# Kernel tuning notes

Hardware: AMD Instinct MI355X
Metric: run time of the kernel (lower is better)

Reference implementation:

```python
import jax, jax.numpy as jnp
import numpy as np

S, B, D, HID, OUT = 96, 16, 512, 128, 2


def setup_inputs() -> dict:
    key = jax.random.key(0)
    ks = jax.random.split(key, 6)
    embeds = jax.random.normal(ks[0], (S, B, D), dtype=jnp.float32)
    embeds_cmp = jax.random.normal(ks[1], (S, B, D), dtype=jnp.float32)
    umask = jnp.ones((B, S), dtype=jnp.float32)   # unused by the math
    qmask = jnp.zeros((S, B, 2), dtype=jnp.float32)  # unused by the math
    # fc: Linear(2*D -> HID); classify: Linear(HID -> OUT)
    W1 = jax.random.normal(ks[2], (HID, 2 * D), dtype=jnp.float32) * 0.02
    b1 = jnp.zeros((HID,), dtype=jnp.float32)
    W2 = jax.random.normal(ks[3], (OUT, HID), dtype=jnp.float32) * 0.02
    b2 = jnp.zeros((OUT,), dtype=jnp.float32)
    return {"embeds": embeds, "umask": umask, "qmask": qmask,
            "embeds_cmp": embeds_cmp, "W1": W1, "b1": b1, "W2": W2, "b2": b2}


def reference(embeds, umask, qmask, embeds_cmp, W1, b1, W2, b2):
    # Pairwise concat [embeds_i ; embeds_cmp_j] -> Linear(2D->HID).
    # Split W1 into halves so the quadratic concat is never materialized:
    # concat(x1,x2) @ W1^T == x1 @ W1a^T + x2 @ W1b^T (same math, fused form).
    d = embeds.shape[-1]
    W1a, W1b = W1[:, :d], W1[:, d:]
    ha = jnp.einsum('ibd,hd->ibh', embeds, W1a)        # [S,B,HID]
    hb = jnp.einsum('jbd,hd->jbh', embeds_cmp, W1b)    # [S,B,HID]
    h = jax.nn.relu(ha[:, None] + hb[None, :] + b1)    # [S,S,B,HID]
    # Dropout(p=0.9) is identity in eval mode.
    logits = jnp.einsum('ijbh,ch->ijbc', h, W2) + b2   # [S,S,B,2]
    return logits
```

## Files before the change

### kernel.cpp

```cpp
#include <hip/hip_runtime.h>

#define S_   96
#define B_   16
#define D_   512
#define HID_ 128
#define M_   (S_ * B_)
#define KC_  4
#define KCH_ (D_ / KC_)
#define CHF_ (2 * M_ * HID_)

typedef __attribute__((ext_vector_type(4))) float        f32x4_t;
typedef __attribute__((ext_vector_type(2))) float        f32x2_t;
typedef __attribute__((ext_vector_type(4))) unsigned int u32x4_t;
typedef __attribute__((ext_vector_type(8))) short        short8;

static __device__ __forceinline__ void split8(f32x4_t a, f32x4_t b,
                                              short8& hi, short8& lo) {
    float f[8];
    #pragma unroll
    for (int j = 0; j < 4; ++j) { f[j] = a[j]; f[4 + j] = b[j]; }
    unsigned int hb[8], lb[8];
    #pragma unroll
    for (int j = 0; j < 8; ++j) {
        unsigned int u = __float_as_uint(f[j]);
        float hf = __uint_as_float(u & 0xffff0000u);
        hb[j] = u >> 16;
        lb[j] = __float_as_uint(f[j] - hf) >> 16;
    }
    union { u32x4_t u; short8 s; } H, L;
    #pragma unroll
    for (int j = 0; j < 4; ++j) {
        H.u[j] = hb[2 * j] | (hb[2 * j + 1] << 16);
        L.u[j] = lb[2 * j] | (lb[2 * j + 1] << 16);
    }
    hi = H.s; lo = L.s;
}

__global__ __launch_bounds__(256) void stage1_mfma(
    const float* __restrict__ emb,
    const float* __restrict__ embc,
    const float* __restrict__ W1,
    const float* __restrict__ b1,
    float* __restrict__ ws)
{
    __shared__ float x_s[64 * 132];
    __shared__ float w_s[64 * 132];

    const int t    = threadIdx.x;
    const int wave = t >> 6;
    const int lane = t & 63;
    const int bx   = blockIdx.x;
    const int h0   = blockIdx.y * 64;
    const int kc   = blockIdx.z;

    const int z    = (bx >= 24) ? 1 : 0;
    const int mloc = bx * 64 - z * M_;

    const float* xbase = (z ? embc : emb) + (size_t)mloc * D_ + kc * KCH_;
    const float* wbase = W1 + (size_t)h0 * (2 * D_) + z * D_ + kc * KCH_;

    #pragma unroll
    for (int rep = 0; rep < 8; ++rep) {
        const int idx = rep * 256 + t;
        const int row = idx >> 5;
        const int c4  = (idx & 31) * 4;
        *(f32x4_t*)&x_s[row * 132 + c4] = *(const f32x4_t*)(xbase + row * D_ + c4);
        *(f32x4_t*)&w_s[row * 132 + c4] = *(const f32x4_t*)(wbase + row * (2 * D_) + c4);
    }
    __syncthreads();

    const int rsel = lane & 15;
    const int kq   = (lane >> 4) * 8;
    const int wm   = (wave & 1) * 32;
    const int wh   = (wave >> 1) * 32;

    f32x4_t acc[2][2] = {{{0.f,0.f,0.f,0.f},{0.f,0.f,0.f,0.f}},
                         {{0.f,0.f,0.f,0.f},{0.f,0.f,0.f,0.f}}};
    #pragma unroll
    for (int kk = 0; kk < KCH_; kk += 32) {
        short8 ahi[2], alo[2], bhi[2], blo[2];
        #pragma unroll
        for (int ms = 0; ms < 2; ++ms) {
            const float* p = &x_s[(wm + ms * 16 + rsel) * 132 + kk + kq];
            split8(*(const f32x4_t*)p, *(const f32x4_t*)(p + 4), ahi[ms], alo[ms]);
        }
        #pragma unroll
        for (int hs = 0; hs < 2; ++hs) {
            const float* p = &w_s[(wh + hs * 16 + rsel) * 132 + kk + kq];
            split8(*(const f32x4_t*)p, *(const f32x4_t*)(p + 4), bhi[hs], blo[hs]);
        }
        #pragma unroll
        for (int ms = 0; ms < 2; ++ms)
            #pragma unroll
            for (int hs = 0; hs < 2; ++hs) {
                acc[ms][hs] = __builtin_amdgcn_mfma_f32_16x16x32_bf16(ahi[ms], bhi[hs], acc[ms][hs], 0, 0, 0);
                acc[ms][hs] = __builtin_amdgcn_mfma_f32_16x16x32_bf16(ahi[ms], blo[hs], acc[ms][hs], 0, 0, 0);
                acc[ms][hs] = __builtin_amdgcn_mfma_f32_16x16x32_bf16(alo[ms], bhi[hs], acc[ms][hs], 0, 0, 0);
            }
    }

    float* dst = ws + (size_t)kc * CHF_ + (size_t)z * (M_ * HID_);
    const int mrow_base = mloc + wm + (lane >> 4) * 4;
    #pragma unroll
    for (int ms = 0; ms < 2; ++ms) {
        #pragma unroll
        for (int hs = 0; hs < 2; ++hs) {
            const int h = h0 + wh + hs * 16 + rsel;
            const float bias = (z == 0 && kc == 0) ? b1[h] : 0.f;
            #pragma unroll
            for (int r = 0; r < 4; ++r) {
                dst[(mrow_base + ms * 16 + r) * HID_ + h] = acc[ms][hs][r] + bias;
            }
        }
    }
}

__global__ __launch_bounds__(256) void stage2(
    const float* __restrict__ ws,
    const float* __restrict__ W2,
    const float* __restrict__ b2,
    float* __restrict__ out)
{
    __shared__ float ha_s[16 * 132];
    __shared__ float hb_s[16 * 132];
    __shared__ float w2_s[2 * HID_];

    const int t  = threadIdx.x;
    const int i0 = blockIdx.x * 16;
    const int j0 = blockIdx.y * 16;
    const int b  = blockIdx.z;

    {
        const int r = t >> 4;
        const int c = (t & 15) * 8;
        const float* pHa = ws + ((i0 + r) * B_ + b) * HID_ + c;
        const float* pHb = ws + (M_ * HID_) + ((j0 + r) * B_ + b) * HID_ + c;
        f32x4_t a0 = *(const f32x4_t*)pHa,  a1  = *(const f32x4_t*)(pHa + 4);
        f32x4_t b0 = *(const f32x4_t*)pHb,  b1v = *(const f32x4_t*)(pHb + 4);
        #pragma unroll
        for (int kc = 1; kc < KC_; ++kc) {
            const float* qa = pHa + (size_t)kc * CHF_;
            const float* qb = pHb + (size_t)kc * CHF_;
            a0  += *(const f32x4_t*)qa;   a1  += *(const f32x4_t*)(qa + 4);
            b0  += *(const f32x4_t*)qb;   b1v += *(const f32x4_t*)(qb + 4);
        }
        *(f32x4_t*)&ha_s[r * 132 + c]     = a0;
        *(f32x4_t*)&ha_s[r * 132 + c + 4] = a1;
        *(f32x4_t*)&hb_s[r * 132 + c]     = b0;
        *(f32x4_t*)&hb_s[r * 132 + c + 4] = b1v;
        w2_s[t] = W2[t];
    }
    __syncthreads();

    const int ti = t >> 4, tj = t & 15;
    const float* pa = &ha_s[ti * 132];
    const float* pb = &hb_s[tj * 132];
    float acc0 = 0.f, acc1 = 0.f;
    #pragma unroll
    for (int h = 0; h < HID_; h += 4) {
        f32x4_t av = *(const f32x4_t*)(pa + h);
        f32x4_t bv = *(const f32x4_t*)(pb + h);
        f32x4_t w0 = *(const f32x4_t*)&w2_s[h];
        f32x4_t w1 = *(const f32x4_t*)&w2_s[HID_ + h];
        #pragma unroll
        for (int q = 0; q < 4; ++q) {
            float v = fmaxf(av[q] + bv[q], 0.f);
            acc0 = fmaf(v, w0[q], acc0);
            acc1 = fmaf(v, w1[q], acc1);
        }
    }

    const int i = i0 + ti, j = j0 + tj;
    const int idx = ((i * S_ + j) * B_ + b) * 2;
    f32x2_t o = { acc0 + b2[0], acc1 + b2[1] };
    *(f32x2_t*)(out + idx) = o;
}

__global__ __launch_bounds__(256) void fused_fallback(
    const float* __restrict__ emb,
    const float* __restrict__ embc,
    const float* __restrict__ W1,
    const float* __restrict__ b1,
    const float* __restrict__ W2,
    const float* __restrict__ b2,
    float* __restrict__ out)
{
    __shared__ float ha_s[16 * 132];
    __shared__ float hb_s[16 * 132];
    __shared__ float w2_s[2 * HID_];

    const int t  = threadIdx.x;
    const int i0 = blockIdx.x * 16;
    const int j0 = blockIdx.y * 16;
    const int b  = blockIdx.z;

    w2_s[t] = W2[t];

    for (int o = t; o < 4096; o += 256) {
        const int side = o >> 11;
        const int mi   = (o >> 7) & 15;
        const int h    = o & 127;
        const int srow = ((side ? j0 : i0) + mi) * B_ + b;
        const float* x = (side ? embc : emb) + srow * D_;
        const float* w = W1 + h * (2 * D_) + side * D_;
        float s = side ? 0.f : b1[h];
        for (int d = 0; d < D_; d += 4) {
            f32x4_t xv = *(const f32x4_t*)(x + d);
            f32x4_t wv = *(const f32x4_t*)(w + d);
            s = fmaf(xv[0], wv[0], s);
            s = fmaf(xv[1], wv[1], s);
            s = fmaf(xv[2], wv[2], s);
            s = fmaf(xv[3], wv[3], s);
        }
        (side ? hb_s : ha_s)[mi * 132 + h] = s;
    }
    __syncthreads();

    const int ti = t >> 4, tj = t & 15;
    const float* pa = &ha_s[ti * 132];
    const float* pb = &hb_s[tj * 132];
    float acc0 = 0.f, acc1 = 0.f;
    #pragma unroll
    for (int h = 0; h < HID_; h += 4) {
        f32x4_t av = *(const f32x4_t*)(pa + h);
        f32x4_t bv = *(const f32x4_t*)(pb + h);
        f32x4_t w0 = *(const f32x4_t*)&w2_s[h];
        f32x4_t w1 = *(const f32x4_t*)&w2_s[HID_ + h];
        #pragma unroll
        for (int q = 0; q < 4; ++q) {
            float v = fmaxf(av[q] + bv[q], 0.f);
            acc0 = fmaf(v, w0[q], acc0);
            acc1 = fmaf(v, w1[q], acc1);
        }
    }
    const int i = i0 + ti, j = j0 + tj;
    const int idx = ((i * S_ + j) * B_ + b) * 2;
    f32x2_t ov = { acc0 + b2[0], acc1 + b2[1] };
    *(f32x2_t*)(out + idx) = ov;
}

extern "C" void kernel_launch(void* const* d_in, const int* in_sizes, int n_in,
                              void* d_out, int out_size, void* d_ws, size_t ws_size,
                              hipStream_t stream) {
    const float* emb  = (const float*)d_in[0];
    const float* embc = (const float*)d_in[3];
    const float* W1   = (const float*)d_in[4];
    const float* b1   = (const float*)d_in[5];
    const float* W2   = (const float*)d_in[6];
    const float* b2   = (const float*)d_in[7];
    float* out = (float*)d_out;

    const size_t need = (size_t)KC_ * CHF_ * sizeof(float);
    if (d_ws != nullptr && ws_size >= need) {
        float* ws = (float*)d_ws;
        stage1_mfma<<<dim3(48, 2, KC_), 256, 0, stream>>>(emb, embc, W1, b1, ws);
        stage2<<<dim3(6, 6, 16), 256, 0, stream>>>(ws, W2, b2, out);
    } else {
        fused_fallback<<<dim3(6, 6, 16), 256, 0, stream>>>(emb, embc, W1, b1, W2, b2, out);
    }
}
```

Measured before the change: 88.21 us.

## Pre-split fp32 tiles into bf16 hi/lo in LDS; read W2 directly from global

```diff
diff --git a/kernel.cpp b/kernel.cpp
--- a/kernel.cpp
+++ b/kernel.cpp
@@ -8,6 +8,7 @@
 #define KC_  4
 #define KCH_ (D_ / KC_)
 #define CHF_ (2 * M_ * HID_)
+#define LSTR_ 136
 
 typedef __attribute__((ext_vector_type(4))) float        f32x4_t;
 typedef __attribute__((ext_vector_type(2))) float        f32x2_t;
@@ -43,8 +44,10 @@
     const float* __restrict__ b1,
     float* __restrict__ ws)
 {
-    __shared__ float x_s[64 * 132];
-    __shared__ float w_s[64 * 132];
+    __shared__ short x_hi[64 * LSTR_];
+    __shared__ short x_lo[64 * LSTR_];
+    __shared__ short w_hi[64 * LSTR_];
+    __shared__ short w_lo[64 * LSTR_];
 
     const int t    = threadIdx.x;
     const int wave = t >> 6;
@@ -60,17 +63,24 @@
     const float* wbase = W1 + (size_t)h0 * (2 * D_) + z * D_ + kc * KCH_;
 
     #pragma unroll
-    for (int rep = 0; rep < 8; ++rep) {
+    for (int rep = 0; rep < 4; ++rep) {
         const int idx = rep * 256 + t;
-        const int row = idx >> 5;
-        const int c4  = (idx & 31) * 4;
-        *(f32x4_t*)&x_s[row * 132 + c4] = *(const f32x4_t*)(xbase + row * D_ + c4);
-        *(f32x4_t*)&w_s[row * 132 + c4] = *(const f32x4_t*)(wbase + row * (2 * D_) + c4);
+        const int row = idx >> 4;
+        const int g   = idx & 15;
+        short8 hi, lo;
+        const float* px = xbase + row * D_ + g * 8;
+        split8(*(const f32x4_t*)px, *(const f32x4_t*)(px + 4), hi, lo);
+        *(short8*)&x_hi[row * LSTR_ + g * 8] = hi;
+        *(short8*)&x_lo[row * LSTR_ + g * 8] = lo;
+        const float* pw = wbase + row * (2 * D_) + g * 8;
+        split8(*(const f32x4_t*)pw, *(const f32x4_t*)(pw + 4), hi, lo);
+        *(short8*)&w_hi[row * LSTR_ + g * 8] = hi;
+        *(short8*)&w_lo[row * LSTR_ + g * 8] = lo;
     }
     __syncthreads();
 
     const int rsel = lane & 15;
-    const int kq   = (lane >> 4) * 8;
+    const int gq   = lane >> 4;
     const int wm   = (wave & 1) * 32;
     const int wh   = (wave >> 1) * 32;
 
@@ -78,16 +88,19 @@
                          {{0.f,0.f,0.f,0.f},{0.f,0.f,0.f,0.f}}};
     #pragma unroll
     for (int kk = 0; kk < KCH_; kk += 32) {
+        const int goff = (kk >> 3) + gq;
         short8 ahi[2], alo[2], bhi[2], blo[2];
         #pragma unroll
         for (int ms = 0; ms < 2; ++ms) {
-            const float* p = &x_s[(wm + ms * 16 + rsel) * 132 + kk + kq];
-            split8(*(const f32x4_t*)p, *(const f32x4_t*)(p + 4), ahi[ms], alo[ms]);
+            const int o = (wm + ms * 16 + rsel) * LSTR_ + goff * 8;
+            ahi[ms] = *(const short8*)&x_hi[o];
+            alo[ms] = *(const short8*)&x_lo[o];
         }
         #pragma unroll
         for (int hs = 0; hs < 2; ++hs) {
-            const float* p = &w_s[(wh + hs * 16 + rsel) * 132 + kk + kq];
-            split8(*(const f32x4_t*)p, *(const f32x4_t*)(p + 4), bhi[hs], blo[hs]);
+            const int o = (wh + hs * 16 + rsel) * LSTR_ + goff * 8;
+            bhi[hs] = *(const short8*)&w_hi[o];
+            blo[hs] = *(const short8*)&w_lo[o];
         }
         #pragma unroll
         for (int ms = 0; ms < 2; ++ms)
@@ -123,7 +136,6 @@
 {
     __shared__ float ha_s[16 * 132];
     __shared__ float hb_s[16 * 132];
-    __shared__ float w2_s[2 * HID_];
 
     const int t  = threadIdx.x;
     const int i0 = blockIdx.x * 16;
@@ -148,7 +160,6 @@
         *(f32x4_t*)&ha_s[r * 132 + c + 4] = a1;
         *(f32x4_t*)&hb_s[r * 132 + c]     = b0;
         *(f32x4_t*)&hb_s[r * 132 + c + 4] = b1v;
-        w2_s[t] = W2[t];
     }
     __syncthreads();
 
@@ -160,8 +171,8 @@
     for (int h = 0; h < HID_; h += 4) {
         f32x4_t av = *(const f32x4_t*)(pa + h);
         f32x4_t bv = *(const f32x4_t*)(pb + h);
-        f32x4_t w0 = *(const f32x4_t*)&w2_s[h];
-        f32x4_t w1 = *(const f32x4_t*)&w2_s[HID_ + h];
+        f32x4_t w0 = *(const f32x4_t*)(W2 + h);
+        f32x4_t w1 = *(const f32x4_t*)(W2 + HID_ + h);
         #pragma unroll
         for (int q = 0; q < 4; ++q) {
             float v = fmaxf(av[q] + bv[q], 0.f);
@@ -187,14 +198,11 @@
 {
     __shared__ float ha_s[16 * 132];
     __shared__ float hb_s[16 * 132];
-    __shared__ float w2_s[2 * HID_];
 
     const int t  = threadIdx.x;
     const int i0 = blockIdx.x * 16;
     const int j0 = blockIdx.y * 16;
     const int b  = blockIdx.z;
-
-    w2_s[t] = W2[t];
 
     for (int o = t; o < 4096; o += 256) {
         const int side = o >> 11;
@@ -224,8 +232,8 @@
     for (int h = 0; h < HID_; h += 4) {
         f32x4_t av = *(const f32x4_t*)(pa + h);
         f32x4_t bv = *(const f32x4_t*)(pb + h);
-        f32x4_t w0 = *(const f32x4_t*)&w2_s[h];
-        f32x4_t w1 = *(const f32x4_t*)&w2_s[HID_ + h];
+        f32x4_t w0 = *(const f32x4_t*)(W2 + h);
+        f32x4_t w1 = *(const f32x4_t*)(W2 + HID_ + h);
         #pragma unroll
         for (int q = 0; q < 4; ++q) {
             float v = fmaxf(av[q] + bv[q], 0.f);
```

Measured after the change: 85.37 us. -3.2%, faster.
